# Kernel optimization log

Hardware: AMD Instinct MI355X
Metric: run time of the kernel (lower is better)

## Reference

```python
import jax, jax.numpy as jnp
import numpy as np
from math import ceil

H, W = 360, 640
H_, W_ = ceil(H / 32) * 32, ceil(W / 32) * 32  # 384, 640
SF = 2
TIMES = [k / SF for k in range(1, SF)]  # [0.5]


def conv(x, w, b=None, pad=1):
    y = jax.lax.conv_general_dilated(x, w, (1, 1), [(pad, pad), (pad, pad)],
                                     dimension_numbers=('NCHW', 'OIHW', 'NCHW'))
    if b is not None:
        y = y + b[None, :, None, None]
    return y


def resize_ac(x, Hn, Wn):
    # bilinear, align_corners=True, NCHW
    B, C, Hs, Ws = x.shape
    if (Hn, Wn) == (Hs, Ws):
        return x
    ys = jnp.linspace(0.0, Hs - 1.0, Hn, dtype=x.dtype)
    xs = jnp.linspace(0.0, Ws - 1.0, Wn, dtype=x.dtype)
    y0 = jnp.floor(ys).astype(jnp.int32); y1 = jnp.minimum(y0 + 1, Hs - 1)
    x0 = jnp.floor(xs).astype(jnp.int32); x1 = jnp.minimum(x0 + 1, Ws - 1)
    wy = (ys - y0)[None, None, :, None]
    wx = (xs - x0)[None, None, None, :]
    rows = x[:, :, y0, :] * (1 - wy) + x[:, :, y1, :] * wy      # [B,C,Hn,Ws]
    return rows[:, :, :, x0] * (1 - wx) + rows[:, :, :, x1] * wx  # [B,C,Hn,Wn]


def warp(img, flow):
    # backward warp with bilinear sampling, zeros padding (grid_sample semantics)
    B, C, Hs, Ws = img.shape
    gy, gx = jnp.meshgrid(jnp.arange(Hs, dtype=img.dtype), jnp.arange(Ws, dtype=img.dtype), indexing='ij')
    xq = gx[None] + flow[:, 0]  # [B,H,W]
    yq = gy[None] + flow[:, 1]

    def samp(im, xx, yy):  # im [C,H,W]
        x0 = jnp.floor(xx).astype(jnp.int32); x1 = x0 + 1
        y0 = jnp.floor(yy).astype(jnp.int32); y1 = y0 + 1
        wx = xx - x0; wy = yy - y0

        def g(xi, yi):
            valid = ((xi >= 0) & (xi < Ws) & (yi >= 0) & (yi < Hs)).astype(im.dtype)
            xc = jnp.clip(xi, 0, Ws - 1); yc = jnp.clip(yi, 0, Hs - 1)
            return im[:, yc, xc] * valid[None]  # [C,H,W] gather

        return (g(x0, y0) * (1 - wx) * (1 - wy) + g(x1, y0) * wx * (1 - wy)
                + g(x0, y1) * (1 - wx) * wy + g(x1, y1) * wx * wy)

    return jax.vmap(samp)(img, xq, yq)


def bmnet(x6, t, w1, b1, w2, b2):
    # stand-in bilateral motion net: conv stack conditioned on time channel -> 2-ch flow
    tch = jnp.full_like(x6[:, :1], t)
    h = jax.nn.relu(conv(jnp.concatenate([x6, tch], 1), w1, b1, 1))
    return conv(h, w2, b2, 1)


def local_expand(x):
    # [B,C,H,W] -> [B,C*9,H,W] of 3x3 neighborhoods (c-major, kernel-position minor)
    B, C, Hs, Ws = x.shape
    xp = jnp.pad(x, ((0, 0), (0, 0), (1, 1), (1, 1)))
    pats = [xp[:, :, dy:dy + Hs, dx:dx + Ws] for dy in range(3) for dx in range(3)]
    return jnp.stack(pats, 2).reshape(B, C * 9, Hs, Ws)


def dynfilter(cand, DF):
    # cand [B,6,H,W], DF [B,54,H,W] -> [B,1,H,W] spatially-varying weighted gather
    pe = local_expand(cand)
    return jnp.einsum('bkhw,bkhw->bhw', pe, DF)[:, None]


def reference(I0, I1, target, ctx_W, bm_W1, bm_b1, bm_W2, bm_b2, df_W1, df_b1, df_W2, df_b2, count):
    tgt = target.at[count].set(I0[0])
    c = count + 1
    pair_r = resize_ac(jnp.concatenate([I0, I1], 1), H_, W_)
    scl = jnp.array([W / W_, H / H_], jnp.float32).reshape(1, 2, 1, 1)
    F01 = resize_ac(bmnet(pair_r, 0.0, bm_W1, bm_b1, bm_W2, bm_b2) * 2.0, H, W) * scl
    F10 = resize_ac(bmnet(pair_r, 1.0, bm_W1, bm_b1, bm_W2, bm_b2) * -2.0, H, W) * scl
    CI0 = jax.nn.relu(conv(I0, ctx_W, None, 3))
    CI1 = jax.nn.relu(conv(I1, ctx_W, None, 3))
    X0 = jnp.concatenate([I0, CI0], 1)  # [1,67,H,W]
    X1 = jnp.concatenate([I1, CI1], 1)
    for t in TIMES:
        ti = 1.0 - t
        BM = resize_ac(bmnet(pair_r, t, bm_W1, bm_b1, bm_W2, bm_b2), H, W) * scl
        C1 = warp(X0, -t * F01)
        C2 = warp(X1, ti * F01)
        C3 = warp(X0, t * F10)
        C4 = warp(X1, (t - 1.0) * F10)
        C5 = warp(X0, BM * (-2.0 * t))
        C6 = warp(X1, BM * (2.0 * ti))
        inp = jnp.concatenate([I0, C1, C2, C3, C4, C5, C6, I1], 1)  # [1,408,H,W]
        h = jax.nn.relu(conv(inp, df_W1, df_b1, 1))
        DF = jax.nn.softmax(conv(h, df_W2, df_b2, 1), axis=1)  # [1,54,H,W]
        cand = inp[:, 3:-3]  # [1,402,H,W]
        R = dynfilter(cand[:, 0::67], DF)
        G = dynfilter(cand[:, 1::67], DF)
        Bc = dynfilter(cand[:, 2::67], DF)
        tgt = tgt.at[c, 0].set(R[0, 0]).at[c, 1].set(G[0, 0]).at[c, 2].set(Bc[0, 0])
        c += 1
    return tgt, c


def setup_inputs() -> dict:
    key = jax.random.key(0)
    ks = jax.random.split(key, 8)
    he = lambda k, shp: jax.random.normal(k, shp, jnp.float32) * np.float32((2.0 / (shp[1] * shp[2] * shp[3])) ** 0.5)
    return {
        'I0': jax.random.uniform(ks[0], (1, 3, H, W), jnp.float32),
        'I1': jax.random.uniform(ks[1], (1, 3, H, W), jnp.float32),
        'target': jnp.zeros((3, 3, H, W), jnp.float32),
        'ctx_W': he(ks[2], (64, 3, 7, 7)),
        'bm_W1': he(ks[3], (32, 7, 3, 3)),
        'bm_b1': jnp.zeros((32,), jnp.float32),
        'bm_W2': he(ks[4], (2, 32, 3, 3)) * np.float32(0.1),  # small flows
        'bm_b2': jnp.zeros((2,), jnp.float32),
        'df_W1': he(ks[5], (32, 408, 3, 3)),
        'df_b1': jnp.zeros((32,), jnp.float32),
        'df_W2': he(ks[6], (54, 32, 3, 3)),
        'df_b2': jnp.zeros((54,), jnp.float32),
        'count': 0,
    }
```

## Files before the change

### kernel.cpp

```cpp
#include <hip/hip_runtime.h>
#include <hip/hip_bf16.h>
#include <hip/hip_fp16.h>

#define Hh 360
#define Ww 640
#define HW (Hh*Ww)
#define Hr 384
#define HWr (Hr*Ww)

#define TW 48
#define TH 4
#define WCOLS 50
#define SROWS 6
#define NXT 14
#define NYT 90
#define NBLK (NXT*NYT)

#define WTW 16
#define WTH 8
#define WCL 18
#define WSR 10
#define WCCH 72
#define WNXT 40
#define WNYT 45
#define WNBLK (WNXT*WNYT)

#define CRS 24

typedef __hip_bfloat16 bf16;
typedef __attribute__((ext_vector_type(8))) short short8v;
typedef __attribute__((ext_vector_type(4))) short short4v;
typedef __attribute__((ext_vector_type(4))) float f32x4;

static __device__ __forceinline__ bf16 f2b(float v) { return __float2bfloat16(v); }
static __device__ __forceinline__ short f2bs(float v) { bf16 t = __float2bfloat16(v); return *(short*)&t; }
static __device__ __forceinline__ float bs2f(short s) {
    unsigned u = ((unsigned)(unsigned short)s) << 16;
    float f; __builtin_memcpy(&f, &u, 4); return f;
}

__global__ void front_all(const float* __restrict__ I0, const float* __restrict__ I1,
                          const float* __restrict__ target, const int* __restrict__ count,
                          const float* __restrict__ dfW1, const float* __restrict__ dfW2,
                          const float* __restrict__ ctxW, const float* __restrict__ bmW2,
                          const float* __restrict__ bmW1,
                          float* __restrict__ out, bf16* __restrict__ I4,
                          bf16* __restrict__ pr8,
                          bf16* __restrict__ wfrag, bf16* __restrict__ wfrag2,
                          bf16* __restrict__ wctx, float* __restrict__ w2t,
                          bf16* __restrict__ wbm1, float* __restrict__ tsW) {
    int idx = blockIdx.x * 256 + threadIdx.x;
    if (idx < 6 * HW + 1) {
        if (idx < 3 * HW) {
            out[idx] = I0[idx];
        } else if (idx < 6 * HW) {
            size_t off = (size_t)6 * HW + (idx - 3 * HW);
            out[off] = target[off];
        } else {
            out[(size_t)9 * HW] = (float)(count[0] + 2);
        }
        return;
    }
    idx -= 6 * HW + 1;
    if (idx < 2 * HW) {
        int z = idx / HW, p = idx % HW;
        const float* img = z ? I1 : I0;
        short4v v;
        v[0] = f2bs(img[p]);
        v[1] = f2bs(img[(size_t)HW + p]);
        v[2] = f2bs(img[(size_t)2 * HW + p]);
        v[3] = 0;
        *(short4v*)((short*)I4 + (size_t)idx * 4) = v;
        return;
    }
    idx -= 2 * HW;
    if (idx < HWr) {
        int p = idx;
        int x = p % Ww, y = p / Ww;
        float ys = y * (359.0f / 383.0f);
        int y0 = (int)floorf(ys);
        if (y0 > 359) y0 = 359;
        int y1 = y0 + 1; if (y1 > 359) y1 = 359;
        float wy = ys - (float)y0;
        short8v v;
        #pragma unroll
        for (int c = 0; c < 6; c++) {
            const float* src = (c < 3) ? (I0 + (size_t)c * HW) : (I1 + (size_t)(c - 3) * HW);
            v[c] = f2bs(src[y0 * Ww + x] * (1.0f - wy) + src[y1 * Ww + x] * wy);
        }
        v[6] = 0; v[7] = 0;
        *(short8v*)((short*)pr8 + (size_t)p * 8) = v;
        return;
    }
    idx -= HWr;
    if (idx < 165888) {
        int j = idx & 7;
        int t = idx >> 3;
        int l = t & 63; t >>= 6;
        int m = t & 1; t >>= 1;
        int chunk = t % 3; t /= 3;
        int q = t % 9;
        int w = t / 9;
        int oc = m * 16 + (l & 15);
        int ch = chunk * 32 + ((l >> 4) << 3) + j;
        int ic = -1;
        if (ch < 67) ic = 3 + 67 * w + ch;
        else if (ch < 70) {
            if (w == 0) ic = ch - 67;
            else if (w == 5) ic = 405 + (ch - 67);
        }
        float v = (ic >= 0) ? dfW1[((oc * 408 + ic) * 3 + q / 3) * 3 + (q % 3)] : 0.0f;
        wfrag[idx] = f2b(v);
        return;
    }
    idx -= 165888;
    if (idx < 18432) {
        int j = idx & 7;
        int t = idx >> 3;
        int l = t & 63; t >>= 6;
        int n = t & 3; t >>= 2;
        int q = t;
        int oc = n * 16 + (l & 15);
        int kch = ((l >> 4) << 3) + j;
        float v = (oc < 54) ? dfW2[((oc * 32 + kch) * 3 + q / 3) * 3 + (q % 3)] : 0.0f;
        wfrag2[idx] = f2b(v);
        return;
    }
    idx -= 18432;
    if (idx < 14336) {
        int j = idx & 7;
        int t = idx >> 3;
        int l = t & 63; t >>= 6;
        int n = t & 3;
        int ky = t >> 2;
        int oc = n * 16 + (l & 15);
        int k = ((l >> 4) << 3) + j;
        int kx = k >> 2, ic = k & 3;
        float v = (kx < 7 && ic < 3) ? ctxW[oc * 147 + ic * 49 + ky * 7 + kx] : 0.0f;
        wctx[idx] = f2b(v);
        return;
    }
    idx -= 14336;
    if (idx < 576) {
        int o = idx & 1;
        int t = idx >> 1;
        int i = t % 32;
        int q = t / 32;
        w2t[idx] = bmW2[o * 288 + i * 9 + q];
        return;
    }
    idx -= 576;
    if (idx < 3072) {
        int j = idx & 7;
        int t = idx >> 3;
        int l = t & 63; t >>= 6;
        int m = t & 1;
        int ky = t >> 1;
        int oc = m * 16 + (l & 15);
        int k = ((l >> 4) << 3) + j;
        int kx = k >> 3, ic = k & 7;
        float v = (kx < 3 && ic < 6) ? bmW1[oc * 63 + ic * 9 + ky * 3 + kx] : 0.0f;
        wbm1[idx] = f2b(v);
        return;
    }
    idx -= 3072;
    if (idx < 288) {
        int o = idx & 31;
        int c = idx >> 5;
        int vy = c / 3, vx = c % 3;
        float s = 0.0f;
        for (int q = 0; q < 9; q++) {
            int ky = q / 3, kx = q % 3;
            bool okY = !((vy == 1 && ky == 0) || (vy == 2 && ky == 2));
            bool okX = !((vx == 1 && kx == 0) || (vx == 2 && kx == 2));
            if (okY && okX) s += bmW1[o * 63 + 54 + q];
        }
        tsW[idx] = s;
    }
}

__global__ __launch_bounds__(256, 4) void bm_base_mfma(const bf16* __restrict__ pr8,
                                                       const bf16* __restrict__ wbm1,
                                                       const float* __restrict__ b1,
                                                       const float* __restrict__ tsW,
                                                       bf16* __restrict__ h) {
    __shared__ short raw8[SROWS * WCOLS * 8];
    __shared__ short outb[192 * 32];
    __shared__ float tsl[288];
    const int tid = threadIdx.x;
    const int bx = blockIdx.x % NXT;
    const int by = blockIdx.x / NXT;
    const int x0 = bx * TW, y0 = by * TH;
    const short8v z8 = {0, 0, 0, 0, 0, 0, 0, 0};

    for (int e = tid; e < 288; e += 256) tsl[e] = tsW[e];
    for (int e = tid; e < SROWS * WCOLS; e += 256) {
        int c = e % WCOLS, r = e / WCOLS;
        int gy = y0 - 1 + r, gx = x0 - 1 + c;
        short8v v = z8;
        if (gy >= 0 && gy < Hr && gx >= 0 && gx < Ww)
            v = *(const short8v*)((const short*)pr8 + ((size_t)gy * Ww + gx) * 8);
        *(short8v*)(raw8 + e * 8) = v;
    }
    __syncthreads();

    const int wv = tid >> 6, lane = tid & 63, l15 = lane & 15, lg = lane >> 4;
    f32x4 acc[3][2];
    {
        float bv0 = b1[l15], bv1 = b1[16 + l15];
        #pragma unroll
        for (int pt = 0; pt < 3; pt++)
            #pragma unroll
            for (int r = 0; r < 4; r++) { acc[pt][0][r] = bv0; acc[pt][1][r] = bv1; }
    }
    #pragma unroll 1
    for (int ky = 0; ky < 3; ky++) {
        short8v bw0 = ((const short8v*)wbm1)[(ky * 2 + 0) * 64 + lane];
        short8v bw1 = ((const short8v*)wbm1)[(ky * 2 + 1) * 64 + lane];
        #pragma unroll
        for (int pt = 0; pt < 3; pt++) {
            int col = pt * 16 + l15;
            short8v a = z8;
            if (lg < 3) a = *(const short8v*)(raw8 + ((wv + ky) * WCOLS + col + lg) * 8);
            acc[pt][0] = __builtin_amdgcn_mfma_f32_16x16x32_bf16(a, bw0, acc[pt][0], 0, 0, 0);
            acc[pt][1] = __builtin_amdgcn_mfma_f32_16x16x32_bf16(a, bw1, acc[pt][1], 0, 0, 0);
        }
    }
    #pragma unroll
    for (int pt = 0; pt < 3; pt++)
        #pragma unroll
        for (int m = 0; m < 2; m++)
            #pragma unroll
            for (int r = 0; r < 4; r++) {
                int px = pt * 16 + (lg << 2) + r;
                outb[(wv * 48 + px) * 32 + m * 16 + l15] = f2bs(acc[pt][m][r]);
            }
    __syncthreads();
    #pragma unroll
    for (int it = 0; it < 3; it++) {
        int e = it * 256 + tid;
        int oc8 = e & 3;
        int px = (e >> 2) % 48;
        int rw = e / 192;
        int gx = x0 + px;
        if (gx < Ww) {
            int gy = y0 + rw;
            short8v bsev = *(const short8v*)(outb + (rw * 48 + px) * 32 + oc8 * 8);
            int vy = (gy == 0) ? 1 : ((gy == Hr - 1) ? 2 : 0);
            int vx = (gx == 0) ? 1 : ((gx == Ww - 1) ? 2 : 0);
            const float* tp = tsl + (vy * 3 + vx) * 32 + oc8 * 8;
            float bsef[8], tsf[8];
            #pragma unroll
            for (int j = 0; j < 8; j++) { bsef[j] = bs2f(bsev[j]); tsf[j] = tp[j]; }
            #pragma unroll
            for (int z = 0; z < 3; z++) {
                float tz = (z == 0) ? 0.0f : ((z == 1) ? 1.0f : 0.5f);
                short8v o;
                #pragma unroll
                for (int j = 0; j < 8; j++)
                    o[j] = f2bs(fmaxf(bsef[j] + tz * tsf[j], 0.0f));
                *(short8v*)((short*)h + ((size_t)z * HWr + (size_t)gy * Ww + gx) * 32 + oc8 * 8) = o;
            }
        }
    }
}

__global__ __launch_bounds__(256) void bm_conv2i(const bf16* __restrict__ h,
                                                 const float* __restrict__ w2t,
                                                 const float* __restrict__ b2,
                                                 float* __restrict__ bmout) {
    int p = blockIdx.x * 256 + threadIdx.x;
    if (p >= HWr) return;
    int z = blockIdx.y;
    int x = p % Ww, y = p / Ww;
    const short* hz = (const short*)h + (size_t)z * HWr * 32;
    float a0 = b2[0], a1 = b2[1];
    for (int ky = 0; ky < 3; ky++) {
        int ny = y + ky - 1;
        if (ny < 0 || ny >= Hr) continue;
        for (int kx = 0; kx < 3; kx++) {
            int nx = x + kx - 1;
            if (nx < 0 || nx >= Ww) continue;
            const float* wp = w2t + (ky * 3 + kx) * 64;
            const short* ip = hz + ((size_t)ny * Ww + nx) * 32;
            #pragma unroll
            for (int ck = 0; ck < 4; ck++) {
                short8v v = *(const short8v*)(ip + ck * 8);
                #pragma unroll
                for (int j = 0; j < 8; j++) {
                    float f = bs2f(v[j]);
                    a0 = fmaf(f, wp[(ck * 8 + j) * 2 + 0], a0);
                    a1 = fmaf(f, wp[(ck * 8 + j) * 2 + 1], a1);
                }
            }
        }
    }
    float f = (z == 0) ? 2.0f : ((z == 1) ? -2.0f : 1.0f);
    bmout[(size_t)(z * 2 + 0) * HWr + p] = a0 * f;
    bmout[(size_t)(z * 2 + 1) * HWr + p] = a1 * f;
}

__global__ __launch_bounds__(256) void flow_resize(const float* __restrict__ bmout,
                                                   float* __restrict__ flows) {
    int p = blockIdx.x * 256 + threadIdx.x;
    if (p >= HW) return;
    int x = p % Ww;
    int y = p / Ww;
    float ys = y * (383.0f / 359.0f);
    int y0 = (int)floorf(ys);
    if (y0 > 383) y0 = 383;
    int y1 = y0 + 1; if (y1 > 383) y1 = 383;
    float wy = ys - (float)y0;
    float o[6];
    #pragma unroll
    for (int zc = 0; zc < 6; zc++) {
        const float* src = bmout + (size_t)zc * HWr;
        float v = src[y0 * Ww + x] * (1.0f - wy) + src[y1 * Ww + x] * wy;
        o[zc] = v * ((zc & 1) ? (360.0f / 384.0f) : 1.0f);
    }
    #pragma unroll
    for (int zc = 0; zc < 6; zc++)
        flows[(size_t)p * 6 + zc] = o[zc];
}

__global__ __launch_bounds__(256, 2) void ctx_mfma(const bf16* __restrict__ I4,
                                                   const bf16* __restrict__ wctx,
                                                   bf16* __restrict__ X) {
    __shared__ short raw4[10 * 54 * 4];
    __shared__ short outb[192 * 72];
    const int tid = threadIdx.x;
    const int z = blockIdx.y;
    const int bx = blockIdx.x % NXT;
    const int by = blockIdx.x / NXT;
    const int x0 = bx * TW, y0 = by * TH;
    const short* img4 = (const short*)I4 + (size_t)z * HW * 4;
    const short4v z4 = {0, 0, 0, 0};

    for (int e = tid; e < 540; e += 256) {
        int c = e % 54, r = e / 54;
        int gy = y0 - 3 + r, gx = x0 - 3 + c;
        short4v v = z4;
        if (gy >= 0 && gy < Hh && gx >= 0 && gx < Ww)
            v = *(const short4v*)(img4 + ((size_t)gy * Ww + gx) * 4);
        *(short4v*)(raw4 + e * 4) = v;
    }
    __syncthreads();

    const int wv = tid >> 6, lane = tid & 63, l15 = lane & 15, lg = lane >> 4;
    f32x4 acc[3][4];
    #pragma unroll
    for (int pt = 0; pt < 3; pt++)
        #pragma unroll
        for (int n = 0; n < 4; n++)
            #pragma unroll
            for (int r = 0; r < 4; r++) acc[pt][n][r] = 0.0f;

    #pragma unroll 1
    for (int ky = 0; ky < 7; ky++) {
        short8v bw[4];
        #pragma unroll
        for (int n = 0; n < 4; n++)
            bw[n] = ((const short8v*)wctx)[(ky * 4 + n) * 64 + lane];
        #pragma unroll
        for (int pt = 0; pt < 3; pt++) {
            int col = pt * 16 + l15;
            int base = ((wv + ky) * 54 + col + 2 * lg) * 4;
            short4v lo = *(const short4v*)(raw4 + base);
            short4v hi = (lg == 3) ? z4 : *(const short4v*)(raw4 + base + 4);
            short8v a = __builtin_shufflevector(lo, hi, 0, 1, 2, 3, 4, 5, 6, 7);
            #pragma unroll
            for (int n = 0; n < 4; n++)
                acc[pt][n] = __builtin_amdgcn_mfma_f32_16x16x32_bf16(a, bw[n], acc[pt][n], 0, 0, 0);
        }
    }

    for (int e = tid; e < 576; e += 256) {
        int ic = e % 3, p = e / 3;
        outb[p * 72 + ic] = raw4[((p / 48 + 3) * 54 + (p % 48) + 3) * 4 + ic];
    }
    for (int e = tid; e < 960; e += 256) {
        int c = e % 5, p = e / 5;
        outb[p * 72 + 67 + c] = 0;
    }
    #pragma unroll
    for (int pt = 0; pt < 3; pt++)
        #pragma unroll
        for (int n = 0; n < 4; n++)
            #pragma unroll
            for (int r = 0; r < 4; r++) {
                int px = pt * 16 + (lg << 2) + r;
                outb[(wv * 48 + px) * 72 + 3 + n * 16 + l15] = f2bs(fmaxf(acc[pt][n][r], 0.0f));
            }
    __syncthreads();
    for (int e = tid; e < 1728; e += 256) {
        int part = e % 9, p = e / 9;
        int gx = x0 + p % 48, gy = y0 + p / 48;
        if (gx < Ww)
            *(short8v*)((short*)X + ((size_t)z * HW + (size_t)gy * Ww + gx) * 72 + part * 8) =
                *(const short8v*)(outb + p * 72 + part * 8);
    }
}

__global__ __launch_bounds__(256, 3) void wdf_all(const bf16* __restrict__ X,
                                                  const float* __restrict__ flows,
                                                  const bf16* __restrict__ wfrag,
                                                  const float* __restrict__ b1,
                                                  const float* __restrict__ I0,
                                                  const float* __restrict__ I1,
                                                  bf16* __restrict__ hdf,
                                                  bf16* __restrict__ candRGB) {
    __shared__ short ldsA[WSR * WCL * WCCH];
    __shared__ short ldsB[WSR * WCL * WCCH];
    const int tid = threadIdx.x;
    const int bid = blockIdx.x;
    const int wg = (bid & 7) * (WNBLK / 8) + (bid >> 3);
    const int bx = wg % WNXT;
    const int by = wg / WNXT;
    const int x0 = bx * WTW, y0 = by * WTH;
    const short8v z8 = {0, 0, 0, 0, 0, 0, 0, 0};

    const int wv = tid >> 6;
    const int lane = tid & 63;
    const int l15 = lane & 15;
    const int lg = lane >> 4;

    auto stage = [&](int w, short* dstb) {
        const int fz = (w < 2) ? 0 : ((w < 4) ? 1 : 2);
        const float fac = ((w < 4) ? 0.5f : 1.0f) *
                          ((w == 1 || w == 2 || w == 5) ? 1.0f : -1.0f);
        const short* xsrc = (const short*)X + (size_t)(w & 1) * HW * 72;
        const float* img = (w == 0) ? I0 : I1;
        int e = tid;
        if (e < WSR * WCL) {
            int c = e % WCL, r = e / WCL;
            int gy = y0 - 1 + r, gx = x0 - 1 + c;
            short* dst = dstb + e * WCCH;
            if (gy < 0 || gy >= Hh || gx < 0 || gx >= Ww) {
                #pragma unroll
                for (int ck = 0; ck < 9; ck++) *(short8v*)(dst + ck * 8) = z8;
            } else {
                int p = gy * Ww + gx;
                float2 fl = *(const float2*)(flows + (size_t)p * 6 + fz * 2);
                float xq = (float)gx + fl.x * fac;
                float yq = (float)gy + fl.y * fac;
                float fx0 = floorf(xq), fy0 = floorf(yq);
                int sx0 = (int)fx0, sy0 = (int)fy0;
                int sx1 = sx0 + 1, sy1 = sy0 + 1;
                float wx = xq - fx0, wy = yq - fy0;
                float vx0 = (sx0 >= 0 && sx0 < Ww) ? 1.0f : 0.0f;
                float vx1 = (sx1 >= 0 && sx1 < Ww) ? 1.0f : 0.0f;
                float vy0 = (sy0 >= 0 && sy0 < Hh) ? 1.0f : 0.0f;
                float vy1 = (sy1 >= 0 && sy1 < Hh) ? 1.0f : 0.0f;
                int cx0 = min(max(sx0, 0), Ww - 1), cx1 = min(max(sx1, 0), Ww - 1);
                int cy0 = min(max(sy0, 0), Hh - 1), cy1 = min(max(sy1, 0), Hh - 1);
                float w00 = (1.0f - wx) * (1.0f - wy) * vx0 * vy0;
                float w10 = wx * (1.0f - wy) * vx1 * vy0;
                float w01 = (1.0f - wx) * wy * vx0 * vy1;
                float w11 = wx * wy * vx1 * vy1;
                const short* s00 = xsrc + ((size_t)cy0 * Ww + cx0) * 72;
                const short* s10 = xsrc + ((size_t)cy0 * Ww + cx1) * 72;
                const short* s01 = xsrc + ((size_t)cy1 * Ww + cx0) * 72;
                const short* s11 = xsrc + ((size_t)cy1 * Ww + cx1) * 72;
                short rgb0 = 0, rgb1 = 0, rgb2 = 0;
                {
                    short8v tA0[5], tA1[5], tA2[5], tA3[5];
                    #pragma unroll
                    for (int ck = 0; ck < 5; ck++) {
                        tA0[ck] = *(const short8v*)(s00 + ck * 8);
                        tA1[ck] = *(const short8v*)(s10 + ck * 8);
                        tA2[ck] = *(const short8v*)(s01 + ck * 8);
                        tA3[ck] = *(const short8v*)(s11 + ck * 8);
                    }
                    #pragma unroll
                    for (int ck = 0; ck < 5; ck++) {
                        short8v o;
                        #pragma unroll
                        for (int j = 0; j < 8; j++) {
                            float v = w00 * bs2f(tA0[ck][j]) + w10 * bs2f(tA1[ck][j]) +
                                      w01 * bs2f(tA2[ck][j]) + w11 * bs2f(tA3[ck][j]);
                            short sv = f2bs(v);
                            o[j] = sv;
                            if (ck == 0 && j == 0) rgb0 = sv;
                            if (ck == 0 && j == 1) rgb1 = sv;
                            if (ck == 0 && j == 2) rgb2 = sv;
                        }
                        *(short8v*)(dst + ck * 8) = o;
                    }
                }
                {
                    short8v tB0[4], tB1[4], tB2[4], tB3[4];
                    #pragma unroll
                    for (int ck = 0; ck < 4; ck++) {
                        tB0[ck] = *(const short8v*)(s00 + 40 + ck * 8);
                        tB1[ck] = *(const short8v*)(s10 + 40 + ck * 8);
                        tB2[ck] = *(const short8v*)(s01 + 40 + ck * 8);
                        tB3[ck] = *(const short8v*)(s11 + 40 + ck * 8);
                    }
                    #pragma unroll
                    for (int ck = 0; ck < 4; ck++) {
                        short8v o;
                        #pragma unroll
                        for (int j = 0; j < 8; j++) {
                            float v = w00 * bs2f(tB0[ck][j]) + w10 * bs2f(tB1[ck][j]) +
                                      w01 * bs2f(tB2[ck][j]) + w11 * bs2f(tB3[ck][j]);
                            o[j] = f2bs(v);
                        }
                        *(short8v*)(dst + 40 + ck * 8) = o;
                    }
                }
                if (w == 0 || w == 5) {
                    dst[67] = f2bs(img[p]);
                    dst[68] = f2bs(img[(size_t)HW + p]);
                    dst[69] = f2bs(img[(size_t)2 * HW + p]);
                }
                if (r >= 1 && r <= WTH && c >= 1 && c <= WTW) {
                    short* crp = (short*)candRGB + (size_t)p * CRS + w * 3;
                    crp[0] = rgb0; crp[1] = rgb1; crp[2] = rgb2;
                }
            }
        }
    };

    f32x4 acc[2][2];
    {
        float bv0 = b1[l15], bv1 = b1[16 + l15];
        #pragma unroll
        for (int rt = 0; rt < 2; rt++)
            #pragma unroll
            for (int r = 0; r < 4; r++) { acc[rt][0][r] = bv0; acc[rt][1][r] = bv1; }
    }

    stage(0, ldsA);
    __syncthreads();

    #pragma unroll 1
    for (int wi = 0; wi < 6; wi++) {
        const int w = (wi < 3) ? (2 * wi) : (2 * (wi - 3) + 1);
        short* curb = (wi & 1) ? ldsB : ldsA;

        const short8v* wf = (const short8v*)(wfrag + (size_t)w * 9 * 3 * 2 * 64 * 8);
        __builtin_amdgcn_s_setprio(1);
        #pragma unroll 1
        for (int ky = 0; ky < 3; ky++) {
            #pragma unroll
            for (int kx = 0; kx < 3; kx++) {
                const int dx = kx - 1;
                const int q = ky * 3 + kx;
                #pragma unroll
                for (int chunk = 0; chunk < 3; chunk++) {
                    short8v bw0 = wf[((q * 3 + chunk) * 2 + 0) * 64 + lane];
                    short8v bw1 = wf[((q * 3 + chunk) * 2 + 1) * 64 + lane];
                    const int koff = (chunk < 2) ? (chunk * 32 + (lg << 3)) : 64;
                    #pragma unroll
                    for (int rt = 0; rt < 2; rt++) {
                        int srow = 2 * wv + rt + ky;
                        int col = 1 + dx + l15;
                        const short8v* apt = (const short8v*)(curb + (srow * WCL + col) * WCCH + koff);
                        short8v a = *apt;
                        acc[rt][0] = __builtin_amdgcn_mfma_f32_16x16x32_bf16(a, bw0, acc[rt][0], 0, 0, 0);
                        acc[rt][1] = __builtin_amdgcn_mfma_f32_16x16x32_bf16(a, bw1, acc[rt][1], 0, 0, 0);
                    }
                }
            }
        }
        __builtin_amdgcn_s_setprio(0);

        if (wi < 5) {
            const int wn = ((wi + 1) < 3) ? (2 * (wi + 1)) : (2 * (wi + 1 - 3) + 1);
            stage(wn, (wi & 1) ? ldsA : ldsB);
        }
        __syncthreads();
    }

    #pragma unroll
    for (int rt = 0; rt < 2; rt++) {
        #pragma unroll
        for (int m = 0; m < 2; m++) {
            #pragma unroll
            for (int r = 0; r < 4; r++) {
                float v = fmaxf(acc[rt][m][r], 0.0f);
                int pxx = (lg << 2) + r;
                ldsA[((2 * wv + rt) * 16 + pxx) * 32 + m * 16 + l15] = f2bs(v);
            }
        }
    }
    __syncthreads();
    #pragma unroll
    for (int it = 0; it < 2; it++) {
        int e = it * 256 + tid;
        int oc8 = e & 3;
        int px = e >> 2;
        int row = px >> 4, xl = px & 15;
        short8v v = *(const short8v*)(ldsA + px * 32 + oc8 * 8);
        *(short8v*)((short*)hdf + ((size_t)(y0 + row) * Ww + x0 + xl) * 32 + oc8 * 8) = v;
    }
}

__global__ __launch_bounds__(256, 3) void df2_mfma(const bf16* __restrict__ hdf,
                                                   const bf16* __restrict__ wf2,
                                                   const float* __restrict__ b2,
                                                   const bf16* __restrict__ candRGB,
                                                   float* __restrict__ out) {
    __shared__ float smem[192 * 65];
    short* sst = (short*)smem;
    const int tid = threadIdx.x;
    const int bx = blockIdx.x % NXT;
    const int by = blockIdx.x / NXT;
    const int x0 = bx * TW, y0 = by * TH;

    const short* hs = (const short*)hdf;
    for (int e = tid; e < SROWS * WCOLS * 4; e += 256) {
        int v = e & 3;
        int c = (e >> 2) % WCOLS;
        int r = e / (4 * WCOLS);
        int gy = y0 - 1 + r, gx = x0 - 1 + c;
        short8v val = {0, 0, 0, 0, 0, 0, 0, 0};
        if (gy >= 0 && gy < Hh && gx >= 0 && gx < Ww)
            val = *(const short8v*)(hs + ((size_t)gy * Ww + gx) * 32 + v * 8);
        *(short8v*)(sst + (r * WCOLS + c) * 32 + v * 8) = val;
    }
    __syncthreads();

    const int wv = tid >> 6, lane = tid & 63, l15 = lane & 15, lg = lane >> 4;
    f32x4 acc[3][4];
    #pragma unroll
    for (int n = 0; n < 4; n++) {
        int oc = n * 16 + l15;
        float bv = (oc < 54) ? b2[oc] : 0.0f;
        #pragma unroll
        for (int pt = 0; pt < 3; pt++)
            #pragma unroll
            for (int r = 0; r < 4; r++) acc[pt][n][r] = bv;
    }
    #pragma unroll 1
    for (int ky = 0; ky < 3; ky++) {
        int srow = wv + ky;
        #pragma unroll
        for (int kx = 0; kx < 3; kx++) {
            int dx = kx - 1, q = ky * 3 + kx;
            short8v bw[4];
            #pragma unroll
            for (int n = 0; n < 4; n++) bw[n] = ((const short8v*)wf2)[(q * 4 + n) * 64 + lane];
            #pragma unroll
            for (int pt = 0; pt < 3; pt++) {
                int col = 1 + pt * 16 + dx + l15;
                short8v a = *(const short8v*)(sst + (srow * WCOLS + col) * 32 + lg * 8);
                #pragma unroll
                for (int n = 0; n < 4; n++)
                    acc[pt][n] = __builtin_amdgcn_mfma_f32_16x16x32_bf16(a, bw[n], acc[pt][n], 0, 0, 0);
            }
        }
    }
    __syncthreads();
    #pragma unroll
    for (int pt = 0; pt < 3; pt++)
        #pragma unroll
        for (int n = 0; n < 4; n++)
            #pragma unroll
            for (int r = 0; r < 4; r++) {
                int px = wv * 48 + pt * 16 + (lg << 2) + r;
                smem[px * 65 + n * 16 + l15] = acc[pt][n][r];
            }
    __syncthreads();

    if (tid < 192) {
        int xl = tid % 48, yl = tid / 48;
        int gx = x0 + xl, gy = y0 + yl;
        if (gx < Ww) {
            const float* lp = smem + tid * 65;
            float m = lp[0];
            #pragma unroll
            for (int o = 1; o < 54; o++) m = fmaxf(m, lp[o]);
            float e[54]; float s = 0.f;
            #pragma unroll
            for (int o = 0; o < 54; o++) { e[o] = __expf(lp[o] - m); s += e[o]; }
            float inv = 1.0f / s;
            float rr = 0, gg = 0, bb = 0;
            const short* cr = (const short*)candRGB;
            #pragma unroll
            for (int dy = 0; dy < 3; dy++) {
                int ny = gy + dy - 1;
                if (ny < 0 || ny >= Hh) continue;
                #pragma unroll
                for (int dx = 0; dx < 3; dx++) {
                    int nx = gx + dx - 1;
                    if (nx < 0 || nx >= Ww) continue;
                    const short* cp = cr + ((size_t)ny * Ww + nx) * CRS;
                    short8v v0 = *(const short8v*)(cp);
                    short8v v1 = *(const short8v*)(cp + 8);
                    short8v v2 = *(const short8v*)(cp + 16);
                    float ch[18];
                    #pragma unroll
                    for (int j = 0; j < 8; j++) { ch[j] = bs2f(v0[j]); ch[8 + j] = bs2f(v1[j]); }
                    ch[16] = bs2f(v2[0]);
                    ch[17] = bs2f(v2[1]);
                    #pragma unroll
                    for (int c6 = 0; c6 < 6; c6++) {
                        float df = e[c6 * 9 + dy * 3 + dx];
                        rr = fmaf(ch[c6 * 3 + 0], df, rr);
                        gg = fmaf(ch[c6 * 3 + 1], df, gg);
                        bb = fmaf(ch[c6 * 3 + 2], df, bb);
                    }
                }
            }
            size_t gp = (size_t)gy * Ww + gx;
            out[(size_t)3 * HW + gp] = rr * inv;
            out[(size_t)4 * HW + gp] = gg * inv;
            out[(size_t)5 * HW + gp] = bb * inv;
        }
    }
}

static inline int cdiv(int a, int b) { return (a + b - 1) / b; }

extern "C" void kernel_launch(void* const* d_in, const int* in_sizes, int n_in,
                              void* d_out, int out_size, void* d_ws, size_t ws_size,
                              hipStream_t stream) {
    const float* I0 = (const float*)d_in[0];
    const float* I1 = (const float*)d_in[1];
    const float* target = (const float*)d_in[2];
    const float* ctx_W = (const float*)d_in[3];
    const float* bm_W1 = (const float*)d_in[4];
    const float* bm_b1 = (const float*)d_in[5];
    const float* bm_W2 = (const float*)d_in[6];
    const float* bm_b2 = (const float*)d_in[7];
    const float* df_W1 = (const float*)d_in[8];
    const float* df_b1 = (const float*)d_in[9];
    const float* df_W2 = (const float*)d_in[10];
    const float* df_b2 = (const float*)d_in[11];
    const int* count = (const int*)d_in[12];
    float* out = (float*)d_out;

    char* ws = (char*)d_ws;
    size_t off = 0;
    auto alloc = [&](size_t bytes) -> char* {
        char* p = ws + off;
        off += (bytes + 255) & ~(size_t)255;
        return p;
    };
    bf16* X = (bf16*)alloc((size_t)2 * HW * 72 * 2);
    float* flows = (float*)alloc((size_t)HW * 6 * 4);
    bf16* candRGB = (bf16*)alloc((size_t)HW * CRS * 2);
    bf16* hdf = (bf16*)alloc((size_t)HW * 32 * 2);
    bf16* I4 = (bf16*)alloc((size_t)2 * HW * 4 * 2);
    bf16* pr8 = (bf16*)alloc((size_t)HWr * 8 * 2);
    float* bmout = (float*)alloc((size_t)6 * HWr * 4);
    bf16* wfrag = (bf16*)alloc((size_t)165888 * 2);
    bf16* wfrag2 = (bf16*)alloc((size_t)18432 * 2);
    bf16* wctx = (bf16*)alloc((size_t)14336 * 2);
    float* w2t = (float*)alloc((size_t)576 * 4);
    bf16* wbm1 = (bf16*)alloc((size_t)3072 * 2);
    float* tsW = (float*)alloc((size_t)288 * 4);
    size_t need = off;
    if (ws_size < need) return;

    bf16* h_bm = (bf16*)X;

    const int FRONT_TOTAL = (6 * HW + 1) + 2 * HW + HWr + 202592;
    front_all<<<cdiv(FRONT_TOTAL, 256), 256, 0, stream>>>(
        I0, I1, target, count, df_W1, df_W2, ctx_W, bm_W2, bm_W1,
        out, I4, pr8, wfrag, wfrag2, wctx, w2t, wbm1, tsW);

    bm_base_mfma<<<NXT * (Hr / TH), 256, 0, stream>>>(pr8, wbm1, bm_b1, tsW, h_bm);
    dim3 g1(cdiv(HWr, 256), 3);
    bm_conv2i<<<g1, 256, 0, stream>>>(h_bm, w2t, bm_b2, bmout);
    flow_resize<<<cdiv(HW, 256), 256, 0, stream>>>(bmout, flows);

    dim3 gc(NBLK, 2);
    ctx_mfma<<<gc, 256, 0, stream>>>(I4, wctx, X);

    wdf_all<<<WNBLK, 256, 0, stream>>>(X, flows, wfrag, df_b1, I0, I1, hdf, candRGB);

    df2_mfma<<<NBLK, 256, 0, stream>>>(hdf, wfrag2, df_b2, candRGB, out);
}
```

Baseline: 270.7 us.

## Store context features as FP8 with separate bf16 RGB plane to shrink gather traffic

The 64 context-feature channels written by ctx_mfma are now encoded as FP8 (e4m3 via hardware packed converts when available), and the RGB channels go to a separate 8-wide bf16 array. wdf_all gathers 16+64 bytes per bilinear tap instead of 144, which cuts the memory traffic of the random-access warp gathers roughly in half. In exchange it adds encode and decode ALU work and loses feature precision. The workspace region is reshaped so the layout still aliases the bm hidden buffer.

Result: faster. 252.7 us (-6.7%).

```diff
diff --git a/kernel.cpp b/kernel.cpp
--- a/kernel.cpp
+++ b/kernel.cpp
@@ -31,12 +31,73 @@
 typedef __attribute__((ext_vector_type(8))) short short8v;
 typedef __attribute__((ext_vector_type(4))) short short4v;
 typedef __attribute__((ext_vector_type(4))) float f32x4;
+typedef __attribute__((ext_vector_type(2))) float f32x2;
+typedef __attribute__((ext_vector_type(4))) int i32x4;
 
 static __device__ __forceinline__ bf16 f2b(float v) { return __float2bfloat16(v); }
 static __device__ __forceinline__ short f2bs(float v) { bf16 t = __float2bfloat16(v); return *(short*)&t; }
 static __device__ __forceinline__ float bs2f(short s) {
     unsigned u = ((unsigned)(unsigned short)s) << 16;
     float f; __builtin_memcpy(&f, &u, 4); return f;
+}
+
+#if defined(__has_builtin)
+#if __has_builtin(__builtin_amdgcn_cvt_pk_f32_fp8) && __has_builtin(__builtin_amdgcn_cvt_pk_fp8_f32)
+#define FP8_HW 1
+#endif
+#endif
+
+static __device__ __forceinline__ void fp8dec4(int dw, float* f) {
+#ifdef FP8_HW
+    f32x2 lo = __builtin_amdgcn_cvt_pk_f32_fp8(dw, false);
+    f32x2 hi = __builtin_amdgcn_cvt_pk_f32_fp8(dw, true);
+    f[0] = lo[0]; f[1] = lo[1]; f[2] = hi[0]; f[3] = hi[1];
+#else
+    #pragma unroll
+    for (int k = 0; k < 4; k++) {
+        int u = (dw >> (8 * k)) & 0xFF;
+        int e = (u >> 3) & 15, m = u & 7;
+        int mant = e ? ((8 + m) << (e - 1)) : m;
+        float v = (float)mant * 0x1p-9f;
+        f[k] = (u & 0x80) ? -v : v;
+    }
+#endif
+}
+
+static __device__ __forceinline__ int fp8enc4(float a, float b, float c, float d) {
+#ifdef FP8_HW
+    int r = __builtin_amdgcn_cvt_pk_fp8_f32(a, b, 0, false);
+    r = __builtin_amdgcn_cvt_pk_fp8_f32(c, d, r, true);
+    return r;
+#else
+    float vals[4] = {a, b, c, d};
+    int r = 0;
+    #pragma unroll
+    for (int k = 0; k < 4; k++) {
+        float v = vals[k];
+        unsigned bits; __builtin_memcpy(&bits, &v, 4);
+        unsigned s = bits >> 31;
+        float av = fabsf(v);
+        int u;
+        if (!(av >= 0x1p-10f)) u = 0;
+        else if (av >= 448.0f) u = 0x7E;
+        else {
+            int e; float fr = frexpf(av, &e);
+            (void)fr;
+            int E = e + 6;
+            if (E < 1) {
+                u = (int)roundf(av * 512.0f);
+            } else {
+                float sc = exp2f((float)(10 - E));
+                int mm = (int)roundf(av * sc) - 8;
+                if (mm == 8) { mm = 0; E++; }
+                u = (E > 15) ? 0x7E : ((E << 3) | mm);
+            }
+        }
+        r |= ((u | (s << 7)) & 0xFF) << (8 * k);
+    }
+    return r;
+#endif
 }
 
 __global__ void front_all(const float* __restrict__ I0, const float* __restrict__ I1,
@@ -325,7 +386,8 @@
 
 __global__ __launch_bounds__(256, 2) void ctx_mfma(const bf16* __restrict__ I4,
                                                    const bf16* __restrict__ wctx,
-                                                   bf16* __restrict__ X) {
+                                                   bf16* __restrict__ Xrgb,
+                                                   unsigned char* __restrict__ Xq) {
     __shared__ short raw4[10 * 54 * 4];
     __shared__ short outb[192 * 72];
     const int tid = threadIdx.x;
@@ -392,16 +454,27 @@
                 outb[(wv * 48 + px) * 72 + 3 + n * 16 + l15] = f2bs(fmaxf(acc[pt][n][r], 0.0f));
             }
     __syncthreads();
-    for (int e = tid; e < 1728; e += 256) {
-        int part = e % 9, p = e / 9;
+    for (int e = tid; e < 960; e += 256) {
+        int part = e % 5, p = e / 5;
         int gx = x0 + p % 48, gy = y0 + p / 48;
-        if (gx < Ww)
-            *(short8v*)((short*)X + ((size_t)z * HW + (size_t)gy * Ww + gx) * 72 + part * 8) =
-                *(const short8v*)(outb + p * 72 + part * 8);
-    }
-}
-
-__global__ __launch_bounds__(256, 3) void wdf_all(const bf16* __restrict__ X,
+        if (gx >= Ww) continue;
+        size_t pix = (size_t)z * HW + (size_t)gy * Ww + gx;
+        if (part == 0) {
+            *(short8v*)((short*)Xrgb + pix * 8) = *(const short8v*)(outb + p * 72);
+        } else {
+            const short* src = outb + p * 72 + 8 + (part - 1) * 16;
+            i32x4 r;
+            #pragma unroll
+            for (int d = 0; d < 4; d++)
+                r[d] = fp8enc4(bs2f(src[4 * d + 0]), bs2f(src[4 * d + 1]),
+                               bs2f(src[4 * d + 2]), bs2f(src[4 * d + 3]));
+            *(i32x4*)(Xq + pix * 64 + (size_t)(part - 1) * 16) = r;
+        }
+    }
+}
+
+__global__ __launch_bounds__(256, 3) void wdf_all(const bf16* __restrict__ Xrgb,
+                                                  const unsigned char* __restrict__ Xq,
                                                   const float* __restrict__ flows,
                                                   const bf16* __restrict__ wfrag,
                                                   const float* __restrict__ b1,
@@ -428,7 +501,8 @@
         const int fz = (w < 2) ? 0 : ((w < 4) ? 1 : 2);
         const float fac = ((w < 4) ? 0.5f : 1.0f) *
                           ((w == 1 || w == 2 || w == 5) ? 1.0f : -1.0f);
-        const short* xsrc = (const short*)X + (size_t)(w & 1) * HW * 72;
+        const short* xrgb = (const short*)Xrgb + (size_t)(w & 1) * HW * 8;
+        const unsigned char* xq = Xq + (size_t)(w & 1) * HW * 64;
         const float* img = (w == 0) ? I0 : I1;
         int e = tid;
         if (e < WSR * WCL) {
@@ -441,12 +515,12 @@
             } else {
                 int p = gy * Ww + gx;
                 float2 fl = *(const float2*)(flows + (size_t)p * 6 + fz * 2);
-                float xq = (float)gx + fl.x * fac;
-                float yq = (float)gy + fl.y * fac;
-                float fx0 = floorf(xq), fy0 = floorf(yq);
+                float xqf = (float)gx + fl.x * fac;
+                float yqf = (float)gy + fl.y * fac;
+                float fx0 = floorf(xqf), fy0 = floorf(yqf);
                 int sx0 = (int)fx0, sy0 = (int)fy0;
                 int sx1 = sx0 + 1, sy1 = sy0 + 1;
-                float wx = xq - fx0, wy = yq - fy0;
+                float wx = xqf - fx0, wy = yqf - fy0;
                 float vx0 = (sx0 >= 0 && sx0 < Ww) ? 1.0f : 0.0f;
                 float vx1 = (sx1 >= 0 && sx1 < Ww) ? 1.0f : 0.0f;
                 float vy0 = (sy0 >= 0 && sy0 < Hh) ? 1.0f : 0.0f;
@@ -457,56 +531,58 @@
                 float w10 = wx * (1.0f - wy) * vx1 * vy0;
                 float w01 = (1.0f - wx) * wy * vx0 * vy1;
                 float w11 = wx * wy * vx1 * vy1;
-                const short* s00 = xsrc + ((size_t)cy0 * Ww + cx0) * 72;
-                const short* s10 = xsrc + ((size_t)cy0 * Ww + cx1) * 72;
-                const short* s01 = xsrc + ((size_t)cy1 * Ww + cx0) * 72;
-                const short* s11 = xsrc + ((size_t)cy1 * Ww + cx1) * 72;
-                short rgb0 = 0, rgb1 = 0, rgb2 = 0;
+                size_t i00 = (size_t)cy0 * Ww + cx0;
+                size_t i10 = (size_t)cy0 * Ww + cx1;
+                size_t i01 = (size_t)cy1 * Ww + cx0;
+                size_t i11 = (size_t)cy1 * Ww + cx1;
+                short8v g00 = *(const short8v*)(xrgb + i00 * 8);
+                short8v g10 = *(const short8v*)(xrgb + i10 * 8);
+                short8v g01 = *(const short8v*)(xrgb + i01 * 8);
+                short8v g11 = *(const short8v*)(xrgb + i11 * 8);
+                const i32x4* q00 = (const i32x4*)(xq + i00 * 64);
+                const i32x4* q10 = (const i32x4*)(xq + i10 * 64);
+                const i32x4* q01 = (const i32x4*)(xq + i01 * 64);
+                const i32x4* q11 = (const i32x4*)(xq + i11 * 64);
+                i32x4 qa[4], qb[4], qc[4], qd[4];
+                #pragma unroll
+                for (int c2 = 0; c2 < 4; c2++) {
+                    qa[c2] = q00[c2]; qb[c2] = q10[c2];
+                    qc[c2] = q01[c2]; qd[c2] = q11[c2];
+                }
+                short rgb0, rgb1, rgb2;
                 {
-                    short8v tA0[5], tA1[5], tA2[5], tA3[5];
+                    short8v o;
                     #pragma unroll
-                    for (int ck = 0; ck < 5; ck++) {
-                        tA0[ck] = *(const short8v*)(s00 + ck * 8);
-                        tA1[ck] = *(const short8v*)(s10 + ck * 8);
-                        tA2[ck] = *(const short8v*)(s01 + ck * 8);
-                        tA3[ck] = *(const short8v*)(s11 + ck * 8);
+                    for (int j = 0; j < 8; j++) {
+                        float v = w00 * bs2f(g00[j]) + w10 * bs2f(g10[j]) +
+                                  w01 * bs2f(g01[j]) + w11 * bs2f(g11[j]);
+                        o[j] = f2bs(v);
                     }
+                    rgb0 = o[0]; rgb1 = o[1]; rgb2 = o[2];
+                    *(short8v*)(dst) = o;
+                }
+                #pragma unroll
+                for (int c2 = 0; c2 < 4; c2++) {
+                    short o16[16];
                     #pragma unroll
-                    for (int ck = 0; ck < 5; ck++) {
-                        short8v o;
+                    for (int d = 0; d < 4; d++) {
+                        float fa[4], fb[4], fc[4], fd[4];
+                        fp8dec4(qa[c2][d], fa);
+                        fp8dec4(qb[c2][d], fb);
+                        fp8dec4(qc[c2][d], fc);
+                        fp8dec4(qd[c2][d], fd);
                         #pragma unroll
-                        for (int j = 0; j < 8; j++) {
-                            float v = w00 * bs2f(tA0[ck][j]) + w10 * bs2f(tA1[ck][j]) +
-                                      w01 * bs2f(tA2[ck][j]) + w11 * bs2f(tA3[ck][j]);
-                            short sv = f2bs(v);
-                            o[j] = sv;
-                            if (ck == 0 && j == 0) rgb0 = sv;
-                            if (ck == 0 && j == 1) rgb1 = sv;
-                            if (ck == 0 && j == 2) rgb2 = sv;
+                        for (int j = 0; j < 4; j++) {
+                            float v = w00 * fa[j] + w10 * fb[j] +
+                                      w01 * fc[j] + w11 * fd[j];
+                            o16[4 * d + j] = f2bs(v);
                         }
-                        *(short8v*)(dst + ck * 8) = o;
                     }
-                }
-                {
-                    short8v tB0[4], tB1[4], tB2[4], tB3[4];
+                    short8v o1, o2;
                     #pragma unroll
-                    for (int ck = 0; ck < 4; ck++) {
-                        tB0[ck] = *(const short8v*)(s00 + 40 + ck * 8);
-                        tB1[ck] = *(const short8v*)(s10 + 40 + ck * 8);
-                        tB2[ck] = *(const short8v*)(s01 + 40 + ck * 8);
-                        tB3[ck] = *(const short8v*)(s11 + 40 + ck * 8);
-                    }
-                    #pragma unroll
-                    for (int ck = 0; ck < 4; ck++) {
-                        short8v o;
-                        #pragma unroll
-                        for (int j = 0; j < 8; j++) {
-                            float v = w00 * bs2f(tB0[ck][j]) + w10 * bs2f(tB1[ck][j]) +
-                                      w01 * bs2f(tB2[ck][j]) + w11 * bs2f(tB3[ck][j]);
-                            o[j] = f2bs(v);
-                        }
-                        *(short8v*)(dst + 40 + ck * 8) = o;
-                    }
+                    for (int j = 0; j < 8; j++) { o1[j] = o16[j]; o2[j] = o16[8 + j]; }
+                    *(short8v*)(dst + 8 + c2 * 16) = o1;
+                    *(short8v*)(dst + 8 + c2 * 16 + 8) = o2;
                 }
                 if (w == 0 || w == 5) {
                     dst[67] = f2bs(img[p]);
@@ -738,7 +814,7 @@
         off += (bytes + 255) & ~(size_t)255;
         return p;
     };
-    bf16* X = (bf16*)alloc((size_t)2 * HW * 72 * 2);
+    char* xreg = alloc((size_t)3 * HWr * 32 * 2);
     float* flows = (float*)alloc((size_t)HW * 6 * 4);
     bf16* candRGB = (bf16*)alloc((size_t)HW * CRS * 2);
     bf16* hdf = (bf16*)alloc((size_t)HW * 32 * 2);
@@ -754,7 +830,9 @@
     size_t need = off;
     if (ws_size < need) return;
 
-    bf16* h_bm = (bf16*)X;
+    bf16* h_bm = (bf16*)xreg;
+    bf16* Xrgb = (bf16*)xreg;
+    unsigned char* Xq = (unsigned char*)(xreg + (size_t)2 * HW * 8 * 2);
 
     const int FRONT_TOTAL = (6 * HW + 1) + 2 * HW + HWr + 202592;
     front_all<<<cdiv(FRONT_TOTAL, 256), 256, 0, stream>>>(
@@ -767,9 +845,9 @@
     flow_resize<<<cdiv(HW, 256), 256, 0, stream>>>(bmout, flows);
 
     dim3 gc(NBLK, 2);
-    ctx_mfma<<<gc, 256, 0, stream>>>(I4, wctx, X);
-
-    wdf_all<<<WNBLK, 256, 0, stream>>>(X, flows, wfrag, df_b1, I0, I1, hdf, candRGB);
+    ctx_mfma<<<gc, 256, 0, stream>>>(I4, wctx, Xrgb, Xq);
+
+    wdf_all<<<WNBLK, 256, 0, stream>>>(Xrgb, Xq, flows, wfrag, df_b1, I0, I1, hdf, candRGB);
 
     df2_mfma<<<NBLK, 256, 0, stream>>>(hdf, wfrag2, df_b2, candRGB, out);
 }
```
